# Kernel optimization log

Hardware: AMD Instinct MI355X
Metric: run time of the kernel (lower is better)

The kernel has to match this reference:

```python
import jax, jax.numpy as jnp
import numpy as np

N = 50_000          # num_nodes
E = 800_000         # num_edges (avg degree 16)
DIMS = [512, 256, 256, 7]   # embedding_dim
SCALING = 2.0


def _glorot(key, shape):
    lim = float(np.sqrt(6.0 / (shape[0] + shape[1])))
    return jax.random.uniform(key, shape, jnp.float32, -lim, lim)


def setup_inputs() -> dict:
    key = jax.random.key(0)
    ks = jax.random.split(key, 16)
    inp = {
        "x": jax.random.normal(ks[0], (N, DIMS[0]), jnp.float32),
        "edge_index": jax.random.randint(ks[1], (2, E), 0, N, dtype=jnp.int32),
        # GCNConv weights (3 layers)
        "W1": _glorot(ks[2], (DIMS[0], DIMS[1])), "b1": jnp.zeros((DIMS[1],), jnp.float32),
        "W2": _glorot(ks[3], (DIMS[1], DIMS[2])), "b2": jnp.zeros((DIMS[2],), jnp.float32),
        "W3": _glorot(ks[4], (DIMS[2], DIMS[3])), "b3": jnp.zeros((DIMS[3],), jnp.float32),
        # pseudo_mlp: Linear(512,512) -> ReLU -> Linear(512,64) -> ReLU -> Linear(64,out)
        "mw1": _glorot(ks[5], (DIMS[0], 512)), "mb1": jnp.zeros((512,), jnp.float32),
        "mw2": _glorot(ks[6], (512, 64)),      "mb2": jnp.zeros((64,), jnp.float32),
        "mw3": _glorot(ks[7], (64, DIMS[-1])), "mb3": jnp.zeros((DIMS[-1],), jnp.float32),
        # parsing_mats[0] (only index 0 is used: learn_soft_edge3 always called with ln=0)
        "parsing0": jnp.ones((DIMS[-1], DIMS[-1]), jnp.float32) / SCALING,
    }
    return inp


def _gcn_conv(h_in, row, col, edge_weight, W, b):
    """PyG-style GCNConv with self-loops, symmetric norm, and per-edge weights."""
    h = h_in @ W                                  # [N, out]
    loop = jnp.arange(N, dtype=row.dtype)
    r = jnp.concatenate([row, loop])
    c = jnp.concatenate([col, loop])
    ew = jnp.concatenate([edge_weight, jnp.ones((N,), h.dtype)])
    deg = jax.ops.segment_sum(ew, c, num_segments=N)
    dinv = jnp.where(deg > 0, jax.lax.rsqrt(jnp.maximum(deg, 1e-12)), 0.0)
    norm = dinv[r] * ew * dinv[c]                 # [E+N]
    out = jax.ops.segment_sum(h[r] * norm[:, None], c, num_segments=N)
    return out + b


def _learn_soft_edge(x, row, col, mw1, mb1, mw2, mb2, mw3, mb3, parsing0):
    # pseudo_mlp logits
    h = jax.nn.relu(x @ mw1 + mb1)
    h = jax.nn.relu(h @ mw2 + mb2)
    logits = h @ mw3 + mb3                        # [N, C]
    s = logits[row]                               # start_logits [E, C]
    e = logits[col]                               # end_logits   [E, C]
    parsing = jax.nn.relu(SCALING * parsing0)     # [C, C]
    # diag(bmm(outer(s,e), P)).sum(-1) == sum_{c,d} s[e,c] * e[e,d] * P[d,c]
    ew = jnp.sum(s * (e @ parsing), axis=1)       # [E]
    mean = ew.mean()
    var = ew.var(ddof=1)                          # torch .var() is unbiased
    return (ew - mean) * jnp.sqrt(1e-4 / var) + 1.0


def reference(x, edge_index, W1, b1, W2, b2, W3, b3,
              mw1, mb1, mw2, mb2, mw3, mb3, parsing0):
    row, col = edge_index[0], edge_index[1]
    ew = _learn_soft_edge(x, row, col, mw1, mb1, mw2, mb2, mw3, mb3, parsing0)
    # layer 0
    h0 = _gcn_conv(x, row, col, ew, W1, b1)       # h = x (saved, pre-ReLU)
    x1 = jax.nn.relu(h0)                          # dropout is identity in eval
    # layer 1 (+ residual to h0)
    x2 = _gcn_conv(x1, row, col, ew, W2, b2)
    x2 = jax.nn.relu(x2) + h0
    # layer 2 (final, no activation)
    out = _gcn_conv(x2, row, col, ew, W3, b3)     # [N, n_classes]
    return out
```

## Files before the change

kernel.cpp:

```cpp
#include <hip/hip_runtime.h>

#define NN 50000
#define EE 800000
#define NB_EDGE 3125
#define NB_E1   1563
#define NB_SCAN 196

typedef __attribute__((ext_vector_type(4))) float f32x4;
typedef __attribute__((ext_vector_type(8))) short bf16x8;
typedef __attribute__((ext_vector_type(8))) unsigned short u16x8;

typedef const __attribute__((address_space(1))) void* gas_p;
typedef __attribute__((address_space(3))) void* las_p;

__device__ __forceinline__ float bf2f(unsigned short u) {
  union { unsigned int i; float f; } v; v.i = ((unsigned int)u) << 16; return v.f;
}
__device__ __forceinline__ unsigned short f2bf(float f) {
  union { float f; unsigned int i; } v; v.f = f;
  unsigned int u = v.i;
  return (unsigned short)((u + 0x7FFFu + ((u >> 16) & 1u)) >> 16);
}

__device__ __forceinline__ int xcd_swizzle(int orig, int nwg) {
  int xcd = orig & 7;
  int pos = orig >> 3;
  int q = nwg >> 3, r = nwg & 7;
  return (xcd < r ? xcd * (q + 1) : r * (q + 1) + (xcd - r) * q) + pos;
}

constexpr size_t O_XBF  = 0;
constexpr size_t O_H1   = O_XBF + 51200000;
constexpr size_t O_G1   = O_H1  + 51200000;
constexpr size_t O_X1   = O_G1  + 25600000;
constexpr size_t O_H2   = O_X1  + 25600000;
constexpr size_t O_LG   = O_H2  + 6400000;
constexpr size_t O_TG   = O_LG  + 1600000;
constexpr size_t O_EWR  = O_TG  + 1600000;
constexpr size_t O_W3P  = O_EWR + 3200000;
constexpr size_t O_CSR  = O_W3P + 3200000;
constexpr size_t O_MW1T = O_CSR + 6400000;
constexpr size_t O_W1T  = O_MW1T + 524288;
constexpr size_t O_W2T  = O_W1T  + 262144;
constexpr size_t O_MW2T = O_W2T  + 131072;
constexpr size_t O_DEG  = O_MW2T + 65536;
constexpr size_t O_CNT  = O_DEG  + 200192;
constexpr size_t O_CUR  = O_CNT  + 200192;
constexpr size_t O_RED  = O_CUR  + 200192;
constexpr size_t O_RPT  = O_RED  + 256;
constexpr size_t O_DINV = O_RPT  + 200192;
constexpr size_t O_BSUM = O_DINV + 200192;

__global__ __launch_bounds__(256) void conv_f2bf4(const float* __restrict__ in,
                                                  unsigned short* __restrict__ out, int n4) {
  int i = blockIdx.x * 256 + threadIdx.x;
  if (i >= n4) return;
  const float4 v = ((const float4*)in)[i];
  ushort4 o; o.x = f2bf(v.x); o.y = f2bf(v.y); o.z = f2bf(v.z); o.w = f2bf(v.w);
  ((ushort4*)out)[i] = o;
}

__global__ __launch_bounds__(256)
void conv_weights(const float* __restrict__ mw1, const float* __restrict__ W1,
                  const float* __restrict__ W2, const float* __restrict__ mw2,
                  const float* __restrict__ W3,
                  unsigned short* __restrict__ mw1t, unsigned short* __restrict__ w1t,
                  unsigned short* __restrict__ w2t, unsigned short* __restrict__ mw2t,
                  float* __restrict__ w3p)
{
  int i = blockIdx.x * 256 + threadIdx.x;
  if (i < 262144) {
    int k = i >> 9, n = i & 511;
    mw1t[(size_t)n * 512 + k] = f2bf(mw1[i]);
  } else if (i < 393216) {
    int j = i - 262144, k = j >> 8, n = j & 255;
    w1t[(size_t)n * 512 + k] = f2bf(W1[j]);
  } else if (i < 458752) {
    int j = i - 393216, k = j >> 8, n = j & 255;
    w2t[(size_t)n * 256 + k] = f2bf(W2[j]);
  } else if (i < 491520) {
    int j = i - 458752, k = j >> 6, n = j & 63;
    mw2t[(size_t)n * 512 + k] = f2bf(mw2[j]);
  } else if (i < 493568) {
    int j = i - 491520, d = j >> 3, c = j & 7;
    w3p[j] = (c < 7) ? W3[d * 7 + c] : 0.f;
  }
}

#define GEMM_STAGE(buf, k0)                                                        \
  _Pragma("unroll")                                                                \
  for (int r = 0; r < 4; ++r) {                                                    \
    const int row = r * 32 + wid * 8 + srow8;                                      \
    int ga = bm + row; ga = ga < M_ ? ga : M_ - 1;                                 \
    int gb = bn + row; gb = gb < N_ ? gb : N_ - 1;                                 \
    __builtin_amdgcn_global_load_lds((gas_p)(pA_ + ((size_t)ga * lda_ + (k0)) * 2 + sks * 16), \
                                     (las_p)(ldsA[buf] + row * 64), 16, 0, 0);     \
    __builtin_amdgcn_global_load_lds((gas_p)(pB_ + ((size_t)gb * ldb_ + (k0)) * 2 + sks * 16), \
                                     (las_p)(ldsB[buf] + row * 64), 16, 0, 0);     \
  }

#define GEMM_BODY(A, lda, Bt, ldb_K, M, Ncols, K, bm, bn)                          \
  __shared__ unsigned short ldsA[2][128 * 64];                                     \
  __shared__ unsigned short ldsB[2][128 * 64];                                     \
  const char* pA_ = (const char*)(A);                                              \
  const char* pB_ = (const char*)(Bt);                                             \
  const int lda_ = (lda), ldb_ = (ldb_K), M_ = (M), N_ = (Ncols);                  \
  const int tid  = threadIdx.x;                                                    \
  const int lane = tid & 63;                                                       \
  const int wid  = tid >> 6;                                                       \
  const int wm   = (wid >> 1) << 6;                                                \
  const int wn   = (wid & 1) << 6;                                                 \
  f32x4 acc[4][4] = {};                                                            \
  const int srow8 = lane >> 3;                                                     \
  const int sks   = (lane & 7) ^ srow8;                                            \
  const int nt    = (K) >> 6;                                                      \
  GEMM_STAGE(0, 0)                                                                 \
  for (int t = 0; t < nt; ++t) {                                                   \
    const int cur = t & 1;                                                         \
    if (t + 1 < nt) {                                                              \
      GEMM_STAGE(cur ^ 1, (t + 1) << 6)                                            \
      asm volatile("s_waitcnt vmcnt(8)" ::: "memory");                             \
    } else {                                                                       \
      asm volatile("s_waitcnt vmcnt(0)" ::: "memory");                             \
    }                                                                              \
    __builtin_amdgcn_s_barrier();                                                  \
    __builtin_amdgcn_sched_barrier(0);                                             \
    const int q   = lane >> 4;                                                     \
    const int r15 = lane & 15;                                                     \
    _Pragma("unroll")                                                              \
    for (int kk = 0; kk < 2; ++kk) {                                               \
      bf16x8 af[4], bfr[4];                                                        \
      _Pragma("unroll")                                                            \
      for (int m = 0; m < 4; ++m) {                                                \
        const int ra = wm + m * 16 + r15;                                          \
        af[m]  = *(const bf16x8*)(ldsA[cur] + ra * 64 + (((kk << 2) + q) ^ (ra & 7)) * 8); \
        const int rb = wn + m * 16 + r15;                                          \
        bfr[m] = *(const bf16x8*)(ldsB[cur] + rb * 64 + (((kk << 2) + q) ^ (rb & 7)) * 8); \
      }                                                                            \
      _Pragma("unroll")                                                            \
      for (int m = 0; m < 4; ++m)                                                  \
        _Pragma("unroll")                                                          \
        for (int n = 0; n < 4; ++n)                                                \
          acc[m][n] = __builtin_amdgcn_mfma_f32_16x16x32_bf16(af[m], bfr[n], acc[m][n], 0, 0, 0); \
    }                                                                              \
    __builtin_amdgcn_sched_barrier(0);                                             \
    __builtin_amdgcn_s_barrier();                                                  \
  }

template<bool RELU, bool BIAS>
__global__ __launch_bounds__(256)
void gemm_bf16(const unsigned short* __restrict__ A, int lda,
               const unsigned short* __restrict__ Bt,
               const float* __restrict__ bias,
               unsigned short* __restrict__ C, int ldc,
               int M, int N, int K)
{
  const int nwg  = gridDim.x * gridDim.y;
  const int wgid = xcd_swizzle(blockIdx.y * gridDim.x + blockIdx.x, nwg);
  const int bn   = (wgid % gridDim.x) << 7;
  const int bm   = (wgid / gridDim.x) << 7;

  GEMM_BODY(A, lda, Bt, K, M, N, K, bm, bn)

  const int q   = lane >> 4;
  const int r15 = lane & 15;
#pragma unroll
  for (int m = 0; m < 4; ++m) {
#pragma unroll
    for (int n = 0; n < 4; ++n) {
      const int gc = bn + wn + n * 16 + r15;
#pragma unroll
      for (int i = 0; i < 4; ++i) {
        const int gr = bm + wm + m * 16 + q * 4 + i;
        if (gr < M && gc < N) {
          float f = acc[m][n][i];
          if (BIAS) f += bias[gc];
          if (RELU) f = fmaxf(f, 0.f);
          C[(size_t)gr * ldc + gc] = f2bf(f);
        }
      }
    }
  }
}

__global__ __launch_bounds__(256)
void gemm_fused(const unsigned short* __restrict__ A,
                const unsigned short* __restrict__ Bt,
                const float* __restrict__ mb1,
                unsigned short* __restrict__ h1,
                unsigned short* __restrict__ g1,
                int M)
{
  const int nwg  = gridDim.x * gridDim.y;
  const int wgid = xcd_swizzle(blockIdx.y * gridDim.x + blockIdx.x, nwg);
  const int bnt  = wgid % gridDim.x;
  const int bn   = bnt << 7;
  const int bm   = (wgid / gridDim.x) << 7;

  GEMM_BODY(A, 512, Bt, 512, M, 768, 512, bm, bn)

  const int q   = lane >> 4;
  const int r15 = lane & 15;
  if (bnt < 4) {
#pragma unroll
    for (int m = 0; m < 4; ++m) {
#pragma unroll
      for (int n = 0; n < 4; ++n) {
        const int gc = bn + wn + n * 16 + r15;
        const float b = mb1[gc];
#pragma unroll
        for (int i = 0; i < 4; ++i) {
          const int gr = bm + wm + m * 16 + q * 4 + i;
          if (gr < M) h1[(size_t)gr * 512 + gc] = f2bf(fmaxf(acc[m][n][i] + b, 0.f));
        }
      }
    }
  } else {
#pragma unroll
    for (int m = 0; m < 4; ++m) {
#pragma unroll
      for (int n = 0; n < 4; ++n) {
        const int gc = bn - 512 + wn + n * 16 + r15;
#pragma unroll
        for (int i = 0; i < 4; ++i) {
          const int gr = bm + wm + m * 16 + q * 4 + i;
          if (gr < M) g1[(size_t)gr * 256 + gc] = f2bf(acc[m][n][i]);
        }
      }
    }
  }
}

__global__ __launch_bounds__(256)
void logits_kernel(const unsigned short* __restrict__ h2, const float* __restrict__ mw3,
                   const float* __restrict__ mb3, const float* __restrict__ par,
                   float* __restrict__ Lg, float* __restrict__ Tg)
{
  __shared__ float w[64 * 8];
  __shared__ float P[64];
  int tid = threadIdx.x;
  for (int i = tid; i < 512; i += 256) {
    int k = i >> 3, c = i & 7;
    w[i] = (c < 7) ? mw3[k * 7 + c] : 0.f;
  }
  if (tid < 64) {
    int d = tid >> 3, c = tid & 7;
    P[tid] = (d < 7 && c < 7) ? fmaxf(2.0f * par[d * 7 + c], 0.f) : 0.f;
  }
  __syncthreads();
  int n = blockIdx.x * 256 + tid;
  if (n >= NN) return;
  const unsigned short* hr = h2 + (size_t)n * 64;
  f32x4 L0 = {0,0,0,0}, L1 = {0,0,0,0};
  for (int k = 0; k < 64; k += 4) {
    ushort4 v = *(const ushort4*)(hr + k);
    float xs[4] = {bf2f(v.x), bf2f(v.y), bf2f(v.z), bf2f(v.w)};
#pragma unroll
    for (int j = 0; j < 4; ++j) {
      L0 += xs[j] * *(const f32x4*)&w[(k + j) * 8];
      L1 += xs[j] * *(const f32x4*)&w[(k + j) * 8 + 4];
    }
  }
  float Ls[8] = {L0[0], L0[1], L0[2], L0[3], L1[0], L1[1], L1[2], 0.f};
#pragma unroll
  for (int c = 0; c < 7; ++c) Ls[c] += mb3[c];
  f32x4 T0 = {0,0,0,0}, T1 = {0,0,0,0};
#pragma unroll
  for (int d = 0; d < 7; ++d) {
    T0 += Ls[d] * *(const f32x4*)&P[d * 8];
    T1 += Ls[d] * *(const f32x4*)&P[d * 8 + 4];
  }
  f32x4 o0 = {Ls[0], Ls[1], Ls[2], Ls[3]};
  f32x4 o1 = {Ls[4], Ls[5], Ls[6], 0.f};
  *(f32x4*)(Lg + (size_t)n * 8)     = o0;
  *(f32x4*)(Lg + (size_t)n * 8 + 4) = o1;
  *(f32x4*)(Tg + (size_t)n * 8)     = T0;
  *(f32x4*)(Tg + (size_t)n * 8 + 4) = T1;
}

__global__ __launch_bounds__(256)
void edge1_kernel(const int* __restrict__ row, const int* __restrict__ col,
                  const float* __restrict__ Lg, const float* __restrict__ Tg,
                  float* __restrict__ ew_raw, int* __restrict__ cnt,
                  double* __restrict__ part)
{
  __shared__ double shs[4], shs2[4];
  const int e0 = blockIdx.x * 512 + threadIdx.x;
  const int e1 = e0 + 256;
  double s = 0.0, s2 = 0.0;
  if (e1 < EE) {
    int r0 = row[e0], c0 = col[e0];
    int r1 = row[e1], c1 = col[e1];
    float4 a00 = *(const float4*)(Lg + (size_t)r0 * 8);
    float4 a01 = *(const float4*)(Lg + (size_t)r0 * 8 + 4);
    float4 a10 = *(const float4*)(Lg + (size_t)r1 * 8);
    float4 a11 = *(const float4*)(Lg + (size_t)r1 * 8 + 4);
    float4 b00 = *(const float4*)(Tg + (size_t)c0 * 8);
    float4 b01 = *(const float4*)(Tg + (size_t)c0 * 8 + 4);
    float4 b10 = *(const float4*)(Tg + (size_t)c1 * 8);
    float4 b11 = *(const float4*)(Tg + (size_t)c1 * 8 + 4);
    float v0 = a00.x*b00.x + a00.y*b00.y + a00.z*b00.z + a00.w*b00.w
             + a01.x*b01.x + a01.y*b01.y + a01.z*b01.z + a01.w*b01.w;
    float v1 = a10.x*b10.x + a10.y*b10.y + a10.z*b10.z + a10.w*b10.w
             + a11.x*b11.x + a11.y*b11.y + a11.z*b11.z + a11.w*b11.w;
    ew_raw[e0] = v0; ew_raw[e1] = v1;
    atomicAdd(&cnt[c0], 1); atomicAdd(&cnt[c1], 1);
    s = (double)v0 + (double)v1;
    s2 = (double)v0 * (double)v0 + (double)v1 * (double)v1;
  } else if (e0 < EE) {
    int r0 = row[e0], c0 = col[e0];
    float4 a00 = *(const float4*)(Lg + (size_t)r0 * 8);
    float4 a01 = *(const float4*)(Lg + (size_t)r0 * 8 + 4);
    float4 b00 = *(const float4*)(Tg + (size_t)c0 * 8);
    float4 b01 = *(const float4*)(Tg + (size_t)c0 * 8 + 4);
    float v0 = a00.x*b00.x + a00.y*b00.y + a00.z*b00.z + a00.w*b00.w
             + a01.x*b01.x + a01.y*b01.y + a01.z*b01.z + a01.w*b01.w;
    ew_raw[e0] = v0;
    atomicAdd(&cnt[c0], 1);
    s = (double)v0; s2 = (double)v0 * (double)v0;
  }
  for (int off = 32; off; off >>= 1) {
    s  += __shfl_down(s, off);
    s2 += __shfl_down(s2, off);
  }
  int wv = threadIdx.x >> 6;
  if ((threadIdx.x & 63) == 0) { shs[wv] = s; shs2[wv] = s2; }
  __syncthreads();
  if (threadIdx.x == 0) {
    part[blockIdx.x]         = shs[0] + shs[1] + shs[2] + shs[3];
    part[NB_E1 + blockIdx.x] = shs2[0] + shs2[1] + shs2[2] + shs2[3];
  }
}

__global__ __launch_bounds__(1024)
void redpart_kernel(const double* __restrict__ part, double* __restrict__ red)
{
  __shared__ double sh[16][2];
  int tid = threadIdx.x;
  double s = 0.0, s2 = 0.0;
  for (int i = tid; i < NB_E1; i += 1024) {
    s  += part[i];
    s2 += part[NB_E1 + i];
  }
  for (int off = 32; off; off >>= 1) {
    s  += __shfl_down(s, off);
    s2 += __shfl_down(s2, off);
  }
  if ((tid & 63) == 0) { sh[tid >> 6][0] = s; sh[tid >> 6][1] = s2; }
  __syncthreads();
  if (tid == 0) {
    double a = 0.0, b = 0.0;
    for (int i = 0; i < 16; ++i) { a += sh[i][0]; b += sh[i][1]; }
    red[0] = a; red[1] = b;
  }
}

__global__ __launch_bounds__(256)
void edge2_kernel(const int* __restrict__ row, const int* __restrict__ col,
                  const float* __restrict__ ew_raw, const double* __restrict__ red,
                  const int* __restrict__ rowptr, int* __restrict__ cursor,
                  float* __restrict__ deg, int2* __restrict__ csr_sw)
{
  int e = blockIdx.x * 256 + threadIdx.x;
  if (e >= EE) return;
  double mean = red[0] / (double)EE;
  double var  = (red[1] - (double)EE * mean * mean) / (double)(EE - 1);
  double scl  = sqrt(1e-4 / var);
  float v = (float)(((double)ew_raw[e] - mean) * scl) + 1.0f;
  int c = col[e];
  atomicAdd(&deg[c], v);
  int pos = atomicAdd(&cursor[c], 1);
  int2 sw; sw.x = row[e]; sw.y = __float_as_int(v);
  csr_sw[rowptr[c] + pos] = sw;
}

__global__ __launch_bounds__(256)
void dinv_kernel(const float* __restrict__ deg, float* __restrict__ dinv)
{
  int n = blockIdx.x * 256 + threadIdx.x;
  if (n >= NN) return;
  float d = deg[n] + 1.0f;
  dinv[n] = d > 0.f ? 1.0f / sqrtf(fmaxf(d, 1e-12f)) : 0.f;
}

__global__ __launch_bounds__(256)
void scale_csr_kernel(int2* __restrict__ csr_sw, const float* __restrict__ dinv)
{
  int i = blockIdx.x * 256 + threadIdx.x;
  if (i >= EE) return;
  int2 sw = csr_sw[i];
  sw.y = __float_as_int(__int_as_float(sw.y) * dinv[sw.x]);
  csr_sw[i] = sw;
}

__global__ __launch_bounds__(256)
void scan1_kernel(const int* __restrict__ cnt, int* __restrict__ bsum)
{
  __shared__ int sh[4];
  int i = blockIdx.x * 256 + threadIdx.x;
  int v = (i < NN) ? cnt[i] : 0;
  for (int off = 32; off; off >>= 1) v += __shfl_down(v, off);
  if ((threadIdx.x & 63) == 0) sh[threadIdx.x >> 6] = v;
  __syncthreads();
  if (threadIdx.x == 0) bsum[blockIdx.x] = sh[0] + sh[1] + sh[2] + sh[3];
}

__global__ __launch_bounds__(256)
void scan2_kernel(int* __restrict__ bsum)
{
  __shared__ int sh[256];
  int tid = threadIdx.x;
  int v = (tid < NB_SCAN) ? bsum[tid] : 0;
  sh[tid] = v;
  __syncthreads();
  for (int off = 1; off < 256; off <<= 1) {
    int t = (tid >= off) ? sh[tid - off] : 0;
    __syncthreads();
    sh[tid] += t;
    __syncthreads();
  }
  if (tid < NB_SCAN) bsum[tid] = sh[tid] - v;
}

__global__ __launch_bounds__(256)
void scan3_kernel(const int* __restrict__ cnt, const int* __restrict__ bsum,
                  int* __restrict__ rowptr)
{
  __shared__ int sh[256];
  int tid = threadIdx.x;
  int i = blockIdx.x * 256 + tid;
  int v = (i < NN) ? cnt[i] : 0;
  sh[tid] = v;
  __syncthreads();
  for (int off = 1; off < 256; off <<= 1) {
    int t = (tid >= off) ? sh[tid - off] : 0;
    __syncthreads();
    sh[tid] += t;
    __syncthreads();
  }
  if (i < NN) rowptr[i + 1] = bsum[blockIdx.x] + sh[tid];
  if (i == 0) rowptr[0] = 0;
}

#define AGG_ACC(sw_, v_)                                                     \
  {                                                                          \
    float w_ = __int_as_float((sw_).y);                                      \
    a0 += w_ * bf2f((v_)[0]); a1 += w_ * bf2f((v_)[1]);                      \
    a2 += w_ * bf2f((v_)[2]); a3 += w_ * bf2f((v_)[3]);                      \
    a4 += w_ * bf2f((v_)[4]); a5 += w_ * bf2f((v_)[5]);                      \
    a6 += w_ * bf2f((v_)[6]); a7 += w_ * bf2f((v_)[7]);                      \
  }

template<int MODE>
__global__ __launch_bounds__(256)
void agg256_kernel(const int* __restrict__ rowptr, const int2* __restrict__ csr_sw,
                   const unsigned short* __restrict__ gsrc,
                   const float* __restrict__ dinv, const float* __restrict__ bias,
                   const unsigned short* __restrict__ h0in,
                   unsigned short* __restrict__ h0out,
                   unsigned short* __restrict__ xout,
                   const float* __restrict__ w3p, float* __restrict__ y3)
{
  int n = blockIdx.x * 4 + (threadIdx.x >> 6);
  if (n >= NN) return;
  const int lane = threadIdx.x & 63;
  const int half = lane >> 5;
  const int l5   = lane & 31;
  const size_t colbase = (size_t)(l5 << 3);

  float a0=0,a1=0,a2=0,a3=0,a4=0,a5=0,a6=0,a7=0;
  const int s = rowptr[n], e = rowptr[n + 1];
  int i = s + half;
  for (; i + 14 < e; i += 16) {
    int2 sw[8];
#pragma unroll
    for (int u = 0; u < 8; ++u) sw[u] = csr_sw[i + 2 * u];
    u16x8 v[8];
#pragma unroll
    for (int u = 0; u < 8; ++u) v[u] = *(const u16x8*)(gsrc + (size_t)sw[u].x * 256 + colbase);
#pragma unroll
    for (int u = 0; u < 8; ++u) AGG_ACC(sw[u], v[u])
  }
  for (; i + 6 < e; i += 8) {
    int2 sw[4];
#pragma unroll
    for (int u = 0; u < 4; ++u) sw[u] = csr_sw[i + 2 * u];
    u16x8 v[4];
#pragma unroll
    for (int u = 0; u < 4; ++u) v[u] = *(const u16x8*)(gsrc + (size_t)sw[u].x * 256 + colbase);
#pragma unroll
    for (int u = 0; u < 4; ++u) AGG_ACC(sw[u], v[u])
  }
  for (; i < e; i += 2) {
    int2 sw = csr_sw[i];
    u16x8 v = *(const u16x8*)(gsrc + (size_t)sw.x * 256 + colbase);
    AGG_ACC(sw, v)
  }
  a0 += __shfl_xor(a0, 32); a1 += __shfl_xor(a1, 32);
  a2 += __shfl_xor(a2, 32); a3 += __shfl_xor(a3, 32);
  a4 += __shfl_xor(a4, 32); a5 += __shfl_xor(a5, 32);
  a6 += __shfl_xor(a6, 32); a7 += __shfl_xor(a7, 32);
  float f0 = half ? a4 : a0;
  float f1 = half ? a5 : a1;
  float f2 = half ? a6 : a2;
  float f3 = half ? a7 : a3;
  const int dbase = (l5 << 3) + (half << 2);
  const float dn = dinv[n];
  const float wd = dn * dn;
  ushort4 sv = *(const ushort4*)(gsrc + (size_t)n * 256 + dbase);
  float4 b = *(const float4*)(bias + dbase);
  f0 = dn * f0 + wd * bf2f(sv.x) + b.x;
  f1 = dn * f1 + wd * bf2f(sv.y) + b.y;
  f2 = dn * f2 + wd * bf2f(sv.z) + b.z;
  f3 = dn * f3 + wd * bf2f(sv.w) + b.w;
  const size_t o = (size_t)n * 256 + dbase;
  if (MODE == 0) {
    ushort4 h;
    h.x = f2bf(f0); h.y = f2bf(f1); h.z = f2bf(f2); h.w = f2bf(f3);
    *(ushort4*)(h0out + o) = h;
    ushort4 xo;
    xo.x = f2bf(fmaxf(f0, 0.f)); xo.y = f2bf(fmaxf(f1, 0.f));
    xo.z = f2bf(fmaxf(f2, 0.f)); xo.w = f2bf(fmaxf(f3, 0.f));
    *(ushort4*)(xout + o) = xo;
  } else {
    ushort4 h = *(const ushort4*)(h0in + o);
    float x0 = bf2f(f2bf(fmaxf(f0, 0.f) + bf2f(h.x)));
    float x1 = bf2f(f2bf(fmaxf(f1, 0.f) + bf2f(h.y)));
    float x2v = bf2f(f2bf(fmaxf(f2, 0.f) + bf2f(h.z)));
    float x3 = bf2f(f2bf(fmaxf(f3, 0.f) + bf2f(h.w)));
    const float* w3r = w3p + (size_t)dbase * 8;
    f32x4 p0 = {0,0,0,0}, p1 = {0,0,0,0};
    p0 += x0 * *(const f32x4*)(w3r +  0); p1 += x0 * *(const f32x4*)(w3r +  4);
    p0 += x1 * *(const f32x4*)(w3r +  8); p1 += x1 * *(const f32x4*)(w3r + 12);
    p0 += x2v * *(const f32x4*)(w3r + 16); p1 += x2v * *(const f32x4*)(w3r + 20);
    p0 += x3 * *(const f32x4*)(w3r + 24); p1 += x3 * *(const f32x4*)(w3r + 28);
#pragma unroll
    for (int off = 1; off < 64; off <<= 1) {
      p0[0] += __shfl_xor(p0[0], off); p0[1] += __shfl_xor(p0[1], off);
      p0[2] += __shfl_xor(p0[2], off); p0[3] += __shfl_xor(p0[3], off);
      p1[0] += __shfl_xor(p1[0], off); p1[1] += __shfl_xor(p1[1], off);
      p1[2] += __shfl_xor(p1[2], off); p1[3] += __shfl_xor(p1[3], off);
    }
    if (lane == 0) {
      *(f32x4*)(y3 + (size_t)n * 8)     = p0;
      *(f32x4*)(y3 + (size_t)n * 8 + 4) = p1;
    }
  }
}

__global__ __launch_bounds__(256)
void agg7_kernel(const int* __restrict__ rowptr, const int2* __restrict__ csr_sw,
                 const float* __restrict__ y3,
                 const float* __restrict__ dinv, const float* __restrict__ b3,
                 float* __restrict__ out)
{
  int n = blockIdx.x * 32 + (threadIdx.x >> 3);
  if (n >= NN) return;
  int j = threadIdx.x & 7;
  float acc = 0.f;
  int s = rowptr[n], e = rowptr[n + 1];
  for (int i = s; i < e; ++i) {
    int2 sw = csr_sw[i];
    acc += __int_as_float(sw.y) * y3[(size_t)sw.x * 8 + j];
  }
  float dn = dinv[n];
  acc = dn * acc + dn * dn * y3[(size_t)n * 8 + j];
  if (j < 7) out[(size_t)n * 7 + j] = acc + b3[j];
}

extern "C" void kernel_launch(void* const* d_in, const int* in_sizes, int n_in,
                              void* d_out, int out_size, void* d_ws, size_t ws_size,
                              hipStream_t stream)
{
  const float* x   = (const float*)d_in[0];
  const int*   ei  = (const int*)d_in[1];
  const float* W1  = (const float*)d_in[2];
  const float* b1  = (const float*)d_in[3];
  const float* W2  = (const float*)d_in[4];
  const float* b2  = (const float*)d_in[5];
  const float* W3  = (const float*)d_in[6];
  const float* b3  = (const float*)d_in[7];
  const float* mw1 = (const float*)d_in[8];
  const float* mb1 = (const float*)d_in[9];
  const float* mw2 = (const float*)d_in[10];
  const float* mb2 = (const float*)d_in[11];
  const float* mw3 = (const float*)d_in[12];
  const float* mb3 = (const float*)d_in[13];
  const float* par = (const float*)d_in[14];
  const int* row = ei;
  const int* col = ei + EE;
  float* out = (float*)d_out;

  char* ws = (char*)d_ws;
  unsigned short* x_bf  = (unsigned short*)(ws + O_XBF);
  unsigned short* h0    = (unsigned short*)(ws + O_XBF);
  unsigned short* h1_bf = (unsigned short*)(ws + O_H1);
  unsigned short* g2_bf = (unsigned short*)(ws + O_H1);
  unsigned short* g1_bf = (unsigned short*)(ws + O_G1);
  unsigned short* x1_bf = (unsigned short*)(ws + O_X1);
  unsigned short* h2_bf = (unsigned short*)(ws + O_H2);
  float* Lg      = (float*)(ws + O_LG);
  float* Tg      = (float*)(ws + O_TG);
  float* ew_raw  = (float*)(ws + O_EWR);
  float* y3      = (float*)(ws + O_EWR);
  float* w3p     = (float*)(ws + O_W3P);
  int2*  csr_sw  = (int2*)(ws + O_CSR);
  double* part   = (double*)(ws + O_CSR);
  unsigned short* mw1t = (unsigned short*)(ws + O_MW1T);
  unsigned short* w1t  = (unsigned short*)(ws + O_W1T);
  unsigned short* w2t  = (unsigned short*)(ws + O_W2T);
  unsigned short* mw2t = (unsigned short*)(ws + O_MW2T);
  float*  deg    = (float*)(ws + O_DEG);
  int*    cnt    = (int*)(ws + O_CNT);
  int*    cursor = (int*)(ws + O_CUR);
  double* red    = (double*)(ws + O_RED);
  int*    rowptr = (int*)(ws + O_RPT);
  float*  dinv   = (float*)(ws + O_DINV);
  int*    bsum   = (int*)(ws + O_BSUM);

  hipMemsetAsync(ws + O_DEG, 0, 3 * 200192, stream);

  conv_f2bf4<<<25000, 256, 0, stream>>>(x, x_bf, NN * 512 / 4);
  conv_weights<<<1929, 256, 0, stream>>>(mw1, W1, W2, mw2, W3, mw1t, w1t, w2t, mw2t, w3p);

  gemm_fused<<<dim3(6, 391), 256, 0, stream>>>(x_bf, mw1t, mb1, h1_bf, g1_bf, NN);
  gemm_bf16<true,  true ><<<dim3(1, 391), 256, 0, stream>>>(h1_bf, 512, mw2t, mb2, h2_bf, 64, NN, 64, 512);
  logits_kernel<<<196, 256, 0, stream>>>(h2_bf, mw3, mb3, par, Lg, Tg);

  edge1_kernel<<<NB_E1, 256, 0, stream>>>(row, col, Lg, Tg, ew_raw, cnt, part);
  redpart_kernel<<<1, 1024, 0, stream>>>(part, red);
  scan1_kernel<<<NB_SCAN, 256, 0, stream>>>(cnt, bsum);
  scan2_kernel<<<1, 256, 0, stream>>>(bsum);
  scan3_kernel<<<NB_SCAN, 256, 0, stream>>>(cnt, bsum, rowptr);
  edge2_kernel<<<NB_EDGE, 256, 0, stream>>>(row, col, ew_raw, red, rowptr, cursor, deg, csr_sw);
  dinv_kernel<<<196, 256, 0, stream>>>(deg, dinv);
  scale_csr_kernel<<<NB_EDGE, 256, 0, stream>>>(csr_sw, dinv);

  agg256_kernel<0><<<12500, 256, 0, stream>>>(rowptr, csr_sw, g1_bf, dinv, b1, nullptr, h0, x1_bf, nullptr, nullptr);
  gemm_bf16<false, false><<<dim3(2, 391), 256, 0, stream>>>(x1_bf, 256, w2t, nullptr, g2_bf, 256, NN, 256, 256);
  agg256_kernel<1><<<12500, 256, 0, stream>>>(rowptr, csr_sw, g2_bf, dinv, b2, h0, nullptr, nullptr, w3p, y3);
  agg7_kernel<<<1563, 256, 0, stream>>>(rowptr, csr_sw, y3, dinv, b3, out);
}
```

Before: 459.6 us.

## Map one half-wave per node in agg256 with grid-stride persistent blocks

The 256-wide aggregation kernel now gives each 32-lane half-wavefront its own node instead of splitting one node's edges across two halves of a 64-lane wave. This removes the cross-half shuffle reduction and halves the shuffle depth in the fused layer-3 projection. Blocks become persistent with a grid-stride loop over nodes (2048 blocks, 8 nodes per block per iteration). Fewer in-flight gathers per node may lengthen per-node latency, and the fixed grid could underuse CUs if occupancy is limited.

```diff
diff --git a/kernel.cpp b/kernel.cpp
--- a/kernel.cpp
+++ b/kernel.cpp
@@ -461,89 +461,98 @@
                    unsigned short* __restrict__ xout,
                    const float* __restrict__ w3p, float* __restrict__ y3)
 {
-  int n = blockIdx.x * 4 + (threadIdx.x >> 6);
-  if (n >= NN) return;
-  const int lane = threadIdx.x & 63;
-  const int half = lane >> 5;
-  const int l5   = lane & 31;
+  const int tid = threadIdx.x;
+  const int hw  = tid >> 5;
+  const int l5  = tid & 31;
   const size_t colbase = (size_t)(l5 << 3);
-
-  float a0=0,a1=0,a2=0,a3=0,a4=0,a5=0,a6=0,a7=0;
-  const int s = rowptr[n], e = rowptr[n + 1];
-  int i = s + half;
-  for (; i + 14 < e; i += 16) {
-    int2 sw[8];
-#pragma unroll
-    for (int u = 0; u < 8; ++u) sw[u] = csr_sw[i + 2 * u];
-    u16x8 v[8];
-#pragma unroll
-    for (int u = 0; u < 8; ++u) v[u] = *(const u16x8*)(gsrc + (size_t)sw[u].x * 256 + colbase);
-#pragma unroll
-    for (int u = 0; u < 8; ++u) AGG_ACC(sw[u], v[u])
-  }
-  for (; i + 6 < e; i += 8) {
-    int2 sw[4];
-#pragma unroll
-    for (int u = 0; u < 4; ++u) sw[u] = csr_sw[i + 2 * u];
-    u16x8 v[4];
-#pragma unroll
-    for (int u = 0; u < 4; ++u) v[u] = *(const u16x8*)(gsrc + (size_t)sw[u].x * 256 + colbase);
-#pragma unroll
-    for (int u = 0; u < 4; ++u) AGG_ACC(sw[u], v[u])
-  }
-  for (; i < e; i += 2) {
-    int2 sw = csr_sw[i];
-    u16x8 v = *(const u16x8*)(gsrc + (size_t)sw.x * 256 + colbase);
-    AGG_ACC(sw, v)
-  }
-  a0 += __shfl_xor(a0, 32); a1 += __shfl_xor(a1, 32);
-  a2 += __shfl_xor(a2, 32); a3 += __shfl_xor(a3, 32);
-  a4 += __shfl_xor(a4, 32); a5 += __shfl_xor(a5, 32);
-  a6 += __shfl_xor(a6, 32); a7 += __shfl_xor(a7, 32);
-  float f0 = half ? a4 : a0;
-  float f1 = half ? a5 : a1;
-  float f2 = half ? a6 : a2;
-  float f3 = half ? a7 : a3;
-  const int dbase = (l5 << 3) + (half << 2);
-  const float dn = dinv[n];
-  const float wd = dn * dn;
-  ushort4 sv = *(const ushort4*)(gsrc + (size_t)n * 256 + dbase);
-  float4 b = *(const float4*)(bias + dbase);
-  f0 = dn * f0 + wd * bf2f(sv.x) + b.x;
-  f1 = dn * f1 + wd * bf2f(sv.y) + b.y;
-  f2 = dn * f2 + wd * bf2f(sv.z) + b.z;
-  f3 = dn * f3 + wd * bf2f(sv.w) + b.w;
-  const size_t o = (size_t)n * 256 + dbase;
-  if (MODE == 0) {
-    ushort4 h;
-    h.x = f2bf(f0); h.y = f2bf(f1); h.z = f2bf(f2); h.w = f2bf(f3);
-    *(ushort4*)(h0out + o) = h;
-    ushort4 xo;
-    xo.x = f2bf(fmaxf(f0, 0.f)); xo.y = f2bf(fmaxf(f1, 0.f));
-    xo.z = f2bf(fmaxf(f2, 0.f)); xo.w = f2bf(fmaxf(f3, 0.f));
-    *(ushort4*)(xout + o) = xo;
-  } else {
-    ushort4 h = *(const ushort4*)(h0in + o);
-    float x0 = bf2f(f2bf(fmaxf(f0, 0.f) + bf2f(h.x)));
-    float x1 = bf2f(f2bf(fmaxf(f1, 0.f) + bf2f(h.y)));
-    float x2v = bf2f(f2bf(fmaxf(f2, 0.f) + bf2f(h.z)));
-    float x3 = bf2f(f2bf(fmaxf(f3, 0.f) + bf2f(h.w)));
-    const float* w3r = w3p + (size_t)dbase * 8;
-    f32x4 p0 = {0,0,0,0}, p1 = {0,0,0,0};
-    p0 += x0 * *(const f32x4*)(w3r +  0); p1 += x0 * *(const f32x4*)(w3r +  4);
-    p0 += x1 * *(const f32x4*)(w3r +  8); p1 += x1 * *(const f32x4*)(w3r + 12);
-    p0 += x2v * *(const f32x4*)(w3r + 16); p1 += x2v * *(const f32x4*)(w3r + 20);
-    p0 += x3 * *(const f32x4*)(w3r + 24); p1 += x3 * *(const f32x4*)(w3r + 28);
-#pragma unroll
-    for (int off = 1; off < 64; off <<= 1) {
-      p0[0] += __shfl_xor(p0[0], off); p0[1] += __shfl_xor(p0[1], off);
-      p0[2] += __shfl_xor(p0[2], off); p0[3] += __shfl_xor(p0[3], off);
-      p1[0] += __shfl_xor(p1[0], off); p1[1] += __shfl_xor(p1[1], off);
-      p1[2] += __shfl_xor(p1[2], off); p1[3] += __shfl_xor(p1[3], off);
-    }
-    if (lane == 0) {
-      *(f32x4*)(y3 + (size_t)n * 8)     = p0;
-      *(f32x4*)(y3 + (size_t)n * 8 + 4) = p1;
+  const int stride = (int)gridDim.x * 8;
+
+  for (int n = blockIdx.x * 8 + hw; n < NN; n += stride) {
+    float a0=0,a1=0,a2=0,a3=0,a4=0,a5=0,a6=0,a7=0;
+    const int s = rowptr[n], e = rowptr[n + 1];
+    int i = s;
+    for (; i + 7 < e; i += 8) {
+      int2 sw[8];
+#pragma unroll
+      for (int u = 0; u < 8; ++u) sw[u] = csr_sw[i + u];
+      u16x8 v[8];
+#pragma unroll
+      for (int u = 0; u < 8; ++u) v[u] = *(const u16x8*)(gsrc + (size_t)sw[u].x * 256 + colbase);
+#pragma unroll
+      for (int u = 0; u < 8; ++u) AGG_ACC(sw[u], v[u])
+    }
+    for (; i + 3 < e; i += 4) {
+      int2 sw[4];
+#pragma unroll
+      for (int u = 0; u < 4; ++u) sw[u] = csr_sw[i + u];
+      u16x8 v[4];
+#pragma unroll
+      for (int u = 0; u < 4; ++u) v[u] = *(const u16x8*)(gsrc + (size_t)sw[u].x * 256 + colbase);
+#pragma unroll
+      for (int u = 0; u < 4; ++u) AGG_ACC(sw[u], v[u])
+    }
+    for (; i < e; ++i) {
+      int2 sw = csr_sw[i];
+      u16x8 v = *(const u16x8*)(gsrc + (size_t)sw.x * 256 + colbase);
+      AGG_ACC(sw, v)
+    }
+    const int dbase = l5 << 3;
+    const float dn = dinv[n];
+    const float wd = dn * dn;
+    u16x8 sv = *(const u16x8*)(gsrc + (size_t)n * 256 + dbase);
+    float4 b0 = *(const float4*)(bias + dbase);
+    float4 b1 = *(const float4*)(bias + dbase + 4);
+    float f0 = dn * a0 + wd * bf2f(sv[0]) + b0.x;
+    float f1 = dn * a1 + wd * bf2f(sv[1]) + b0.y;
+    float f2 = dn * a2 + wd * bf2f(sv[2]) + b0.z;
+    float f3 = dn * a3 + wd * bf2f(sv[3]) + b0.w;
+    float f4 = dn * a4 + wd * bf2f(sv[4]) + b1.x;
+    float f5 = dn * a5 + wd * bf2f(sv[5]) + b1.y;
+    float f6 = dn * a6 + wd * bf2f(sv[6]) + b1.z;
+    float f7 = dn * a7 + wd * bf2f(sv[7]) + b1.w;
+    const size_t o = (size_t)n * 256 + dbase;
+    if (MODE == 0) {
+      u16x8 h;
+      h[0] = f2bf(f0); h[1] = f2bf(f1); h[2] = f2bf(f2); h[3] = f2bf(f3);
+      h[4] = f2bf(f4); h[5] = f2bf(f5); h[6] = f2bf(f6); h[7] = f2bf(f7);
+      *(u16x8*)(h0out + o) = h;
+      u16x8 xo;
+      xo[0] = f2bf(fmaxf(f0, 0.f)); xo[1] = f2bf(fmaxf(f1, 0.f));
+      xo[2] = f2bf(fmaxf(f2, 0.f)); xo[3] = f2bf(fmaxf(f3, 0.f));
+      xo[4] = f2bf(fmaxf(f4, 0.f)); xo[5] = f2bf(fmaxf(f5, 0.f));
+      xo[6] = f2bf(fmaxf(f6, 0.f)); xo[7] = f2bf(fmaxf(f7, 0.f));
+      *(u16x8*)(xout + o) = xo;
+    } else {
+      u16x8 h = *(const u16x8*)(h0in + o);
+      float xv0 = bf2f(f2bf(fmaxf(f0, 0.f) + bf2f(h[0])));
+      float xv1 = bf2f(f2bf(fmaxf(f1, 0.f) + bf2f(h[1])));
+      float xv2 = bf2f(f2bf(fmaxf(f2, 0.f) + bf2f(h[2])));
+      float xv3 = bf2f(f2bf(fmaxf(f3, 0.f) + bf2f(h[3])));
+      float xv4 = bf2f(f2bf(fmaxf(f4, 0.f) + bf2f(h[4])));
+      float xv5 = bf2f(f2bf(fmaxf(f5, 0.f) + bf2f(h[5])));
+      float xv6 = bf2f(f2bf(fmaxf(f6, 0.f) + bf2f(h[6])));
+      float xv7 = bf2f(f2bf(fmaxf(f7, 0.f) + bf2f(h[7])));
+      const float* w3r = w3p + (size_t)dbase * 8;
+      f32x4 p0 = {0,0,0,0}, p1 = {0,0,0,0};
+      p0 += xv0 * *(const f32x4*)(w3r +  0); p1 += xv0 * *(const f32x4*)(w3r +  4);
+      p0 += xv1 * *(const f32x4*)(w3r +  8); p1 += xv1 * *(const f32x4*)(w3r + 12);
+      p0 += xv2 * *(const f32x4*)(w3r + 16); p1 += xv2 * *(const f32x4*)(w3r + 20);
+      p0 += xv3 * *(const f32x4*)(w3r + 24); p1 += xv3 * *(const f32x4*)(w3r + 28);
+      p0 += xv4 * *(const f32x4*)(w3r + 32); p1 += xv4 * *(const f32x4*)(w3r + 36);
+      p0 += xv5 * *(const f32x4*)(w3r + 40); p1 += xv5 * *(const f32x4*)(w3r + 44);
+      p0 += xv6 * *(const f32x4*)(w3r + 48); p1 += xv6 * *(const f32x4*)(w3r + 52);
+      p0 += xv7 * *(const f32x4*)(w3r + 56); p1 += xv7 * *(const f32x4*)(w3r + 60);
+#pragma unroll
+      for (int off = 1; off < 32; off <<= 1) {
+        p0[0] += __shfl_xor(p0[0], off); p0[1] += __shfl_xor(p0[1], off);
+        p0[2] += __shfl_xor(p0[2], off); p0[3] += __shfl_xor(p0[3], off);
+        p1[0] += __shfl_xor(p1[0], off); p1[1] += __shfl_xor(p1[1], off);
+        p1[2] += __shfl_xor(p1[2], off); p1[3] += __shfl_xor(p1[3], off);
+      }
+      if (l5 == 0) {
+        *(f32x4*)(y3 + (size_t)n * 8)     = p0;
+        *(f32x4*)(y3 + (size_t)n * 8 + 4) = p1;
+      }
     }
   }
 }
@@ -636,8 +645,8 @@
   dinv_kernel<<<196, 256, 0, stream>>>(deg, dinv);
   scale_csr_kernel<<<NB_EDGE, 256, 0, stream>>>(csr_sw, dinv);
 
-  agg256_kernel<0><<<12500, 256, 0, stream>>>(rowptr, csr_sw, g1_bf, dinv, b1, nullptr, h0, x1_bf, nullptr, nullptr);
+  agg256_kernel<0><<<2048, 256, 0, stream>>>(rowptr, csr_sw, g1_bf, dinv, b1, nullptr, h0, x1_bf, nullptr, nullptr);
   gemm_bf16<false, false><<<dim3(2, 391), 256, 0, stream>>>(x1_bf, 256, w2t, nullptr, g2_bf, 256, NN, 256, 256);
-  agg256_kernel<1><<<12500, 256, 0, stream>>>(rowptr, csr_sw, g2_bf, dinv, b2, h0, nullptr, nullptr, w3p, y3);
+  agg256_kernel<1><<<2048, 256, 0, stream>>>(rowptr, csr_sw, g2_bf, dinv, b2, h0, nullptr, nullptr, w3p, y3);
   agg7_kernel<<<1563, 256, 0, stream>>>(rowptr, csr_sw, y3, dinv, b3, out);
 }
```

Result: faster. 441.8 us (-3.9%).
